# Optimization experiments

Hardware: AMD Instinct MI355X
Metric: run time of the kernel (lower is better)

## Reference

```python
import jax, jax.numpy as jnp
import numpy as np

NUM_HEADS = 24
HEAD_DIM = 128
DIM = NUM_HEADS * HEAD_DIM  # 3072
EPS = 1e-6


def rms_norm(x, g):
    # x: [b, h, s, d], g: [d]
    var = jnp.mean(jnp.square(x.astype(jnp.float32)), axis=-1, keepdims=True)
    return (x.astype(jnp.float32) * jax.lax.rsqrt(var + EPS)).astype(x.dtype) * g


def apply_rope(x, cos, sin):
    # x: [b, h, s, d]; cos/sin: [s, d//2]; complex multiply on interleaved pairs
    b, h, s, d = x.shape
    xr = x.reshape(b, h, s, d // 2, 2)
    x0, x1 = xr[..., 0], xr[..., 1]
    c = cos[None, None, :, :]
    sn = sin[None, None, :, :]
    o0 = x0 * c - x1 * sn
    o1 = x0 * sn + x1 * c
    return jnp.stack([o0, o1], axis=-1).reshape(b, h, s, d)


def split_heads(x):
    # [b, s, h*d] -> [b, h, s, d]
    b, s, _ = x.shape
    return x.reshape(b, s, NUM_HEADS, HEAD_DIM).transpose(0, 2, 1, 3)


def setup_inputs() -> dict:
    key = jax.random.key(0)
    ks = jax.random.split(key, 16)
    b, s_img, s_txt = 1, 2048, 256
    image = jax.random.normal(ks[0], (b, s_img, DIM), jnp.float32)
    text = jax.random.normal(ks[1], (b, s_txt, DIM), jnp.float32)
    # rotary freqs: angles = pos * inv_freq
    half = HEAD_DIM // 2
    inv_freq = 1.0 / (10000.0 ** (np.arange(half, dtype=np.float32) / half))
    ang_i = np.arange(s_img, dtype=np.float32)[:, None] * inv_freq[None, :]
    ang_t = np.arange(s_txt, dtype=np.float32)[:, None] * inv_freq[None, :]
    img_cos, img_sin = jnp.cos(jnp.asarray(ang_i)), jnp.sin(jnp.asarray(ang_i))
    txt_cos, txt_sin = jnp.cos(jnp.asarray(ang_t)), jnp.sin(jnp.asarray(ang_t))
    sc = 1.0 / np.sqrt(DIM)
    Wqkv = jax.random.normal(ks[2], (DIM, 3 * DIM), jnp.float32) * sc
    bqkv = jnp.zeros((3 * DIM,), jnp.float32)
    Wadd = jax.random.normal(ks[3], (DIM, 3 * DIM), jnp.float32) * sc
    badd = jnp.zeros((3 * DIM,), jnp.float32)
    gq = jnp.ones((HEAD_DIM,), jnp.float32)
    gk = jnp.ones((HEAD_DIM,), jnp.float32)
    gaq = jnp.ones((HEAD_DIM,), jnp.float32)
    gak = jnp.ones((HEAD_DIM,), jnp.float32)
    Wout = jax.random.normal(ks[4], (DIM, DIM), jnp.float32) * sc
    bout = jnp.zeros((DIM,), jnp.float32)
    Waddout = jax.random.normal(ks[5], (DIM, DIM), jnp.float32) * sc
    baddout = jnp.zeros((DIM,), jnp.float32)
    return dict(image=image, text=text, img_cos=img_cos, img_sin=img_sin,
                txt_cos=txt_cos, txt_sin=txt_sin, Wqkv=Wqkv, bqkv=bqkv,
                Wadd=Wadd, badd=badd, gq=gq, gk=gk, gaq=gaq, gak=gak,
                Wout=Wout, bout=bout, Waddout=Waddout, baddout=baddout)


def reference(image, text, img_cos, img_sin, txt_cos, txt_sin,
              Wqkv, bqkv, Wadd, badd, gq, gk, gaq, gak,
              Wout, bout, Waddout, baddout):
    seq_txt = text.shape[1]
    img_qkv = image @ Wqkv + bqkv
    img_q, img_k, img_v = jnp.split(img_qkv, 3, axis=-1)
    txt_qkv = text @ Wadd + badd
    txt_q, txt_k, txt_v = jnp.split(txt_qkv, 3, axis=-1)

    img_q, img_k, img_v = split_heads(img_q), split_heads(img_k), split_heads(img_v)
    txt_q, txt_k, txt_v = split_heads(txt_q), split_heads(txt_k), split_heads(txt_v)

    img_q, img_k = rms_norm(img_q, gq), rms_norm(img_k, gk)
    txt_q, txt_k = rms_norm(txt_q, gaq), rms_norm(txt_k, gak)

    img_q = apply_rope(img_q, img_cos, img_sin)
    img_k = apply_rope(img_k, img_cos, img_sin)
    txt_q = apply_rope(txt_q, txt_cos, txt_sin)
    txt_k = apply_rope(txt_k, txt_cos, txt_sin)

    # joint attention: text tokens first, then image tokens
    q = jnp.concatenate([txt_q, img_q], axis=2)  # [b, h, S, d]
    k = jnp.concatenate([txt_k, img_k], axis=2)
    v = jnp.concatenate([txt_v, img_v], axis=2)

    scale = 1.0 / np.sqrt(HEAD_DIM)
    scores = jnp.einsum('bhqd,bhkd->bhqk', q, k) * scale
    probs = jax.nn.softmax(scores, axis=-1)
    attn = jnp.einsum('bhqk,bhkd->bhqd', probs, v)
    b, h, S, d = attn.shape
    attn = attn.transpose(0, 2, 1, 3).reshape(b, S, h * d)  # [b, S, dim]

    txt_out = attn[:, :seq_txt, :]
    img_out = attn[:, seq_txt:, :]
    img_out = img_out @ Wout + bout
    txt_out = txt_out @ Waddout + baddout
    return img_out, txt_out
```

## Files before the change

### kernel.cpp

```cpp
#include <hip/hip_runtime.h>

#define NH 24
#define HD 128
#define DM 3072
#define DM3 9216
#define STXT 256
#define SIMG 2048
#define SALL 2304

typedef __attribute__((ext_vector_type(8))) short bfrag;
typedef __attribute__((ext_vector_type(4))) float ffrag;

__device__ __forceinline__ unsigned short f2bf(float f) {
  unsigned int x = __builtin_bit_cast(unsigned int, f);
  x += 0x7fffu + ((x >> 16) & 1u);
  return (unsigned short)(x >> 16);
}

__device__ __forceinline__ void gload16(void* lds, const void* g) {
  __builtin_amdgcn_global_load_lds((const __attribute__((address_space(1))) unsigned int*)g,
                                   (__attribute__((address_space(3))) unsigned int*)lds, 16, 0, 0);
}

__global__ __launch_bounds__(256) void cast_kernel(const float* __restrict__ in,
                                                   unsigned short* __restrict__ out) {
  int i = blockIdx.x * 256 + threadIdx.x;
  float4 a = ((const float4*)in)[2 * i];
  float4 b = ((const float4*)in)[2 * i + 1];
  uint4 o;
  o.x = (unsigned)f2bf(a.x) | ((unsigned)f2bf(a.y) << 16);
  o.y = (unsigned)f2bf(a.z) | ((unsigned)f2bf(a.w) << 16);
  o.z = (unsigned)f2bf(b.x) | ((unsigned)f2bf(b.y) << 16);
  o.w = (unsigned)f2bf(b.z) | ((unsigned)f2bf(b.w) << 16);
  ((uint4*)out)[i] = o;
}

__global__ __launch_bounds__(256) void transpose_cast_kernel(const float* __restrict__ W,
                                                             unsigned short* __restrict__ Wt,
                                                             int K, int N) {
  __shared__ __align__(16) unsigned short tile[64 * 72];
  int k0 = blockIdx.y * 64, n0 = blockIdx.x * 64;
  int t = threadIdx.x;
  int rr = t >> 4, cc = (t & 15) * 4;
#pragma unroll
  for (int p = 0; p < 4; ++p) {
    int k = rr + p * 16;
    float4 v = *(const float4*)&W[(size_t)(k0 + k) * N + n0 + cc];
    tile[(cc + 0) * 72 + k] = f2bf(v.x);
    tile[(cc + 1) * 72 + k] = f2bf(v.y);
    tile[(cc + 2) * 72 + k] = f2bf(v.z);
    tile[(cc + 3) * 72 + k] = f2bf(v.w);
  }
  __syncthreads();
  int n = t >> 2, c = (t & 3) * 16;
  float4* dst = (float4*)&Wt[(size_t)(n0 + n) * K + k0 + c];
  dst[0] = *(float4*)&tile[n * 72 + c];
  dst[1] = *(float4*)&tile[n * 72 + c + 8];
}

__global__ __launch_bounds__(256) void gemm_bt(const unsigned short* __restrict__ A,
                                               const unsigned short* __restrict__ Bt,
                                               const float* __restrict__ bias,
                                               int M, int N, int K, int mode,
                                               float* __restrict__ outf,
                                               unsigned short* __restrict__ outb, int s_off) {
  __shared__ __align__(16) unsigned short As[128 * 32];
  __shared__ __align__(16) unsigned short Bs[128 * 32];
  const int tid = threadIdx.x;
  const int wave = tid >> 6, lane = tid & 63, quad = lane >> 4, l16 = lane & 15;
  const int wm = (wave >> 1) * 64, wn = (wave & 1) * 64;
  const size_t m0 = (size_t)blockIdx.y * 128, n0 = (size_t)blockIdx.x * 128;

  ffrag zf = {0.f, 0.f, 0.f, 0.f};
  ffrag acc[4][4];
#pragma unroll
  for (int i = 0; i < 4; ++i)
#pragma unroll
    for (int j = 0; j < 4; ++j) acc[i][j] = zf;

  const int sr = tid >> 2;
  const int sc = (tid & 3) * 8;
  const unsigned short* Ag0 = A + (m0 + sr) * K + sc;
  const unsigned short* Bg0 = Bt + (n0 + sr) * K + sc;
  unsigned short* Ad0 = &As[sr * 32 + sc];
  unsigned short* Ad1 = &As[(sr + 64) * 32 + sc];
  unsigned short* Bd0 = &Bs[sr * 32 + sc];
  unsigned short* Bd1 = &Bs[(sr + 64) * 32 + sc];

  for (int k0 = 0; k0 < K; k0 += 32) {
    __syncthreads();
    gload16(Ad0, Ag0 + k0);
    gload16(Ad1, Ag0 + (size_t)64 * K + k0);
    gload16(Bd0, Bg0 + k0);
    gload16(Bd1, Bg0 + (size_t)64 * K + k0);
    __syncthreads();
    bfrag af[4], bfv[4];
#pragma unroll
    for (int mt = 0; mt < 4; ++mt)
      af[mt] = *(const bfrag*)&As[(wm + mt * 16 + l16) * 32 + quad * 8];
#pragma unroll
    for (int nt = 0; nt < 4; ++nt)
      bfv[nt] = *(const bfrag*)&Bs[(wn + nt * 16 + l16) * 32 + quad * 8];
#pragma unroll
    for (int mt = 0; mt < 4; ++mt)
#pragma unroll
      for (int nt = 0; nt < 4; ++nt)
        acc[mt][nt] = __builtin_amdgcn_mfma_f32_16x16x32_bf16(af[mt], bfv[nt], acc[mt][nt], 0, 0, 0);
  }

  float bv[4];
#pragma unroll
  for (int nt = 0; nt < 4; ++nt) bv[nt] = bias[n0 + wn + nt * 16 + l16];

#pragma unroll
  for (int mt = 0; mt < 4; ++mt) {
#pragma unroll
    for (int nt = 0; nt < 4; ++nt) {
      int gn = (int)n0 + wn + nt * 16 + l16;
#pragma unroll
      for (int r = 0; r < 4; ++r) {
        float v = acc[mt][nt][r] + bv[nt];
        int gm = (int)m0 + wm + mt * 16 + quad * 4 + r;
        if (mode == 2) {
          outf[(size_t)gm * N + gn] = v;
        } else {
          int which = gn / DM;
          int rr2 = gn - which * DM;
          int head = rr2 >> 7, d = rr2 & 127;
          int s = s_off + gm;
          if (which < 2)
            outf[(((size_t)which * NH + head) * SALL + s) * HD + d] = v;
          else
            outb[((size_t)head * HD + d) * SALL + s] = f2bf(v);
        }
      }
    }
  }
}

__global__ __launch_bounds__(256) void norm_rope_kernel(
    const float* __restrict__ qkvf, const float* __restrict__ gq, const float* __restrict__ gk,
    const float* __restrict__ gaq, const float* __restrict__ gak,
    const float* __restrict__ img_cos, const float* __restrict__ img_sin,
    const float* __restrict__ txt_cos, const float* __restrict__ txt_sin,
    unsigned short* __restrict__ Qb, unsigned short* __restrict__ Kb) {
  int wave = threadIdx.x >> 6, lane = threadIdx.x & 63;
  int row = blockIdx.x * 4 + wave;
  int which = row / (NH * SALL);
  int rem = row - which * (NH * SALL);
  int s = rem % SALL;
  float2 v = *(const float2*)&qkvf[(size_t)row * HD + lane * 2];
  float ss = v.x * v.x + v.y * v.y;
#pragma unroll
  for (int m = 1; m < 64; m <<= 1) ss += __shfl_xor(ss, m);
  float rinv = rsqrtf(ss * (1.0f / 128.0f) + 1e-6f);
  bool is_txt = s < STXT;
  int pos = is_txt ? s : s - STXT;
  const float* g = (which == 0) ? (is_txt ? gaq : gq) : (is_txt ? gak : gk);
  const float* ct = is_txt ? txt_cos : img_cos;
  const float* st = is_txt ? txt_sin : img_sin;
  float c = ct[pos * 64 + lane], sn = st[pos * 64 + lane];
  float x0 = v.x * rinv * g[lane * 2];
  float x1 = v.y * rinv * g[lane * 2 + 1];
  float o0 = x0 * c - x1 * sn;
  float o1 = x0 * sn + x1 * c;
  unsigned short* out = (which == 0 ? Qb : Kb) + (size_t)rem * HD + lane * 2;
  *(unsigned int*)out = (unsigned)f2bf(o0) | ((unsigned)f2bf(o1) << 16);
}

__global__ __launch_bounds__(256) void flash_kernel(const unsigned short* __restrict__ Q,
                                                    const unsigned short* __restrict__ Kg,
                                                    const unsigned short* __restrict__ Vt,
                                                    unsigned short* __restrict__ attn) {
  __shared__ __align__(16) unsigned short Kl[64 * 128];
  __shared__ __align__(16) unsigned short Vl[128 * 64];
  __shared__ __align__(16) unsigned short Pl[4 * 16 * 64];
  int bid = blockIdx.x;
  int g = (bid & 7) * 108 + (bid >> 3);
  const int h = g / 36;
  const int qb = (g - h * 36) * 64;
  const int tid = threadIdx.x;
  const int wave = tid >> 6, lane = tid & 63, quad = lane >> 4, l16 = lane & 15;
  const int l7 = l16 & 7;

  const unsigned short* qrow = Q + ((size_t)h * SALL + qb + wave * 16 + l16) * HD;
  bfrag aq[4];
#pragma unroll
  for (int kk = 0; kk < 4; ++kk) aq[kk] = *(const bfrag*)&qrow[kk * 32 + quad * 8];

  const unsigned short* Kh = Kg + (size_t)h * SALL * HD;
  const unsigned short* Vh = Vt + (size_t)h * HD * SALL;

  const int kr = tid >> 4, kc = tid & 15;
  const int vr = tid >> 3, vc = tid & 7;
  const int kswz = kc ^ (kr & 7);
  const int vswz = vc ^ (vr & 7);

  ffrag zf = {0.f, 0.f, 0.f, 0.f};
  ffrag o[8];
#pragma unroll
  for (int i = 0; i < 8; ++i) o[i] = zf;
  float m_r[4] = {-__builtin_inff(), -__builtin_inff(), -__builtin_inff(), -__builtin_inff()};
  float l_r[4] = {0.f, 0.f, 0.f, 0.f};
  const float sc = 0.08838834764831845f * 1.4426950408889634f;

  bfrag kreg[4], vreg[4];
#pragma unroll
  for (int p = 0; p < 4; ++p) {
    kreg[p] = *(const bfrag*)&Kh[(size_t)(kr + p * 16) * HD + kc * 8];
    vreg[p] = *(const bfrag*)&Vh[(size_t)(vr + p * 32) * SALL + vc * 8];
  }

  for (int t = 0; t < SALL / 64; ++t) {
    __syncthreads();
#pragma unroll
    for (int p = 0; p < 4; ++p) {
      *(bfrag*)&Kl[(kr + p * 16) * 128 + kswz * 8] = kreg[p];
      *(bfrag*)&Vl[(vr + p * 32) * 64 + vswz * 8] = vreg[p];
    }
    __syncthreads();

    if (t + 1 < SALL / 64) {
      int kn = (t + 1) * 64;
#pragma unroll
      for (int p = 0; p < 4; ++p) {
        kreg[p] = *(const bfrag*)&Kh[(size_t)(kn + kr + p * 16) * HD + kc * 8];
        vreg[p] = *(const bfrag*)&Vh[(size_t)(vr + p * 32) * SALL + kn + vc * 8];
      }
    }

    ffrag s_[4];
#pragma unroll
    for (int nt = 0; nt < 4; ++nt) s_[nt] = zf;
#pragma unroll
    for (int kk = 0; kk < 4; ++kk) {
#pragma unroll
      for (int nt = 0; nt < 4; ++nt) {
        bfrag kf = *(const bfrag*)&Kl[(nt * 16 + l16) * 128 + ((kk * 4 + quad) ^ l7) * 8];
        s_[nt] = __builtin_amdgcn_mfma_f32_16x16x32_bf16(aq[kk], kf, s_[nt], 0, 0, 0);
      }
    }
#pragma unroll
    for (int nt = 0; nt < 4; ++nt)
#pragma unroll
      for (int r = 0; r < 4; ++r) s_[nt][r] *= sc;

    float alpha[4];
#pragma unroll
    for (int r = 0; r < 4; ++r) {
      float mx = fmaxf(fmaxf(s_[0][r], s_[1][r]), fmaxf(s_[2][r], s_[3][r]));
#pragma unroll
      for (int msk = 1; msk < 16; msk <<= 1) mx = fmaxf(mx, __shfl_xor(mx, msk));
      float mnew = fmaxf(m_r[r], mx);
      alpha[r] = exp2f(m_r[r] - mnew);
      m_r[r] = mnew;
      float rs = 0.f;
#pragma unroll
      for (int nt = 0; nt < 4; ++nt) {
        float p = exp2f(s_[nt][r] - mnew);
        s_[nt][r] = p;
        rs += p;
      }
#pragma unroll
      for (int msk = 1; msk < 16; msk <<= 1) rs += __shfl_xor(rs, msk);
      l_r[r] = l_r[r] * alpha[r] + rs;
    }
#pragma unroll
    for (int dt = 0; dt < 8; ++dt)
#pragma unroll
      for (int r = 0; r < 4; ++r) o[dt][r] *= alpha[r];
#pragma unroll
    for (int r = 0; r < 4; ++r) {
      int prow = quad * 4 + r;
#pragma unroll
      for (int nt = 0; nt < 4; ++nt)
        Pl[wave * 1024 + prow * 64 + ((nt * 16 + l16) ^ ((prow & 7) << 3))] = f2bf(s_[nt][r]);
    }

    bfrag pf0 = *(const bfrag*)&Pl[wave * 1024 + l16 * 64 + ((quad)     ^ l7) * 8];
    bfrag pf1 = *(const bfrag*)&Pl[wave * 1024 + l16 * 64 + ((quad + 4) ^ l7) * 8];
#pragma unroll
    for (int dt = 0; dt < 8; ++dt) {
      bfrag vf0 = *(const bfrag*)&Vl[(dt * 16 + l16) * 64 + ((quad)     ^ l7) * 8];
      bfrag vf1 = *(const bfrag*)&Vl[(dt * 16 + l16) * 64 + ((quad + 4) ^ l7) * 8];
      o[dt] = __builtin_amdgcn_mfma_f32_16x16x32_bf16(pf0, vf0, o[dt], 0, 0, 0);
      o[dt] = __builtin_amdgcn_mfma_f32_16x16x32_bf16(pf1, vf1, o[dt], 0, 0, 0);
    }
  }

  float linv[4];
#pragma unroll
  for (int r = 0; r < 4; ++r) linv[r] = 1.0f / l_r[r];
#pragma unroll
  for (int dt = 0; dt < 8; ++dt) {
#pragma unroll
    for (int r = 0; r < 4; ++r) {
      int s = qb + wave * 16 + quad * 4 + r;
      attn[(size_t)s * DM + h * HD + dt * 16 + l16] = f2bf(o[dt][r] * linv[r]);
    }
  }
}

extern "C" void kernel_launch(void* const* d_in, const int* in_sizes, int n_in,
                              void* d_out, int out_size, void* d_ws, size_t ws_size,
                              hipStream_t stream) {
  const float* image = (const float*)d_in[0];
  const float* text = (const float*)d_in[1];
  const float* img_cos = (const float*)d_in[2];
  const float* img_sin = (const float*)d_in[3];
  const float* txt_cos = (const float*)d_in[4];
  const float* txt_sin = (const float*)d_in[5];
  const float* Wqkv = (const float*)d_in[6];
  const float* bqkv = (const float*)d_in[7];
  const float* Wadd = (const float*)d_in[8];
  const float* badd = (const float*)d_in[9];
  const float* gq = (const float*)d_in[10];
  const float* gk = (const float*)d_in[11];
  const float* gaq = (const float*)d_in[12];
  const float* gak = (const float*)d_in[13];
  const float* Wout = (const float*)d_in[14];
  const float* bout = (const float*)d_in[15];
  const float* Waddout = (const float*)d_in[16];
  const float* baddout = (const float*)d_in[17];

  char* ws = (char*)d_ws;
  size_t off = 0;
  unsigned short* img_bf = (unsigned short*)(ws + off); off += (size_t)SIMG * DM * 2;
  unsigned short* txt_bf = (unsigned short*)(ws + off); off += (size_t)STXT * DM * 2;
  unsigned short* attn = img_bf;
  unsigned short* Wqkv_t = (unsigned short*)(ws + off); off += (size_t)DM3 * DM * 2;
  unsigned short* Wadd_t = (unsigned short*)(ws + off); off += (size_t)DM3 * DM * 2;
  unsigned short* Wout_t = (unsigned short*)(ws + off); off += (size_t)DM * DM * 2;
  unsigned short* Waddout_t = (unsigned short*)(ws + off); off += (size_t)DM * DM * 2;
  float* qkvf = (float*)(ws + off); off += (size_t)2 * NH * SALL * HD * 4;
  unsigned short* Qb = (unsigned short*)(ws + off); off += (size_t)NH * SALL * HD * 2;
  unsigned short* Kb = (unsigned short*)(ws + off); off += (size_t)NH * SALL * HD * 2;
  unsigned short* Vtb = (unsigned short*)(ws + off); off += (size_t)NH * HD * SALL * 2;
  if (off > ws_size) return;

  cast_kernel<<<SIMG * DM / 2048, 256, 0, stream>>>(image, img_bf);
  cast_kernel<<<STXT * DM / 2048, 256, 0, stream>>>(text, txt_bf);
  transpose_cast_kernel<<<dim3(DM3 / 64, DM / 64), 256, 0, stream>>>(Wqkv, Wqkv_t, DM, DM3);
  transpose_cast_kernel<<<dim3(DM3 / 64, DM / 64), 256, 0, stream>>>(Wadd, Wadd_t, DM, DM3);
  transpose_cast_kernel<<<dim3(DM / 64, DM / 64), 256, 0, stream>>>(Wout, Wout_t, DM, DM);
  transpose_cast_kernel<<<dim3(DM / 64, DM / 64), 256, 0, stream>>>(Waddout, Waddout_t, DM, DM);

  gemm_bt<<<dim3(DM3 / 128, SIMG / 128), 256, 0, stream>>>(img_bf, Wqkv_t, bqkv, SIMG, DM3, DM,
                                                           0, qkvf, Vtb, STXT);
  gemm_bt<<<dim3(DM3 / 128, STXT / 128), 256, 0, stream>>>(txt_bf, Wadd_t, badd, STXT, DM3, DM,
                                                           0, qkvf, Vtb, 0);

  norm_rope_kernel<<<2 * NH * SALL / 4, 256, 0, stream>>>(qkvf, gq, gk, gaq, gak, img_cos,
                                                          img_sin, txt_cos, txt_sin, Qb, Kb);

  flash_kernel<<<dim3(SALL / 64 * NH), 256, 0, stream>>>(Qb, Kb, Vtb, attn);

  gemm_bt<<<dim3(DM / 128, SIMG / 128), 256, 0, stream>>>(attn + (size_t)STXT * DM, Wout_t, bout,
                                                          SIMG, DM, DM, 2, (float*)d_out, nullptr, 0);
  gemm_bt<<<dim3(DM / 128, STXT / 128), 256, 0, stream>>>(attn, Waddout_t, baddout, STXT, DM, DM,
                                                          2, (float*)d_out + (size_t)SIMG * DM,
                                                          nullptr, 0);
}
```

Measured before the change: 1.031 ms.

## Replace 128x128 GEMM with double-buffered 256x256 tile kernel merging text/image launches

Replaces the 128x128 single-buffered bf16 GEMM with a 512-thread 256x256 tile kernel. It uses a 64-wide K step, double-buffered LDS fills via global_load_lds, a swizzled LDS layout, and interleaved MFMA phases with barriers and setprio. Text and image rows are stored contiguously, so each projection pair runs as one launch: the first 256-row block (text) selects the text weights and bias, and the rest use the image weights. The aim is more operand reuse, overlap of memory loads with MFMA work, and fewer launches. The trade-offs are higher register and LDS pressure and fewer blocks per launch.

```diff
diff --git a/kernel.cpp b/kernel.cpp
--- a/kernel.cpp
+++ b/kernel.cpp
@@ -58,80 +58,154 @@
   dst[1] = *(float4*)&tile[n * 72 + c + 8];
 }
 
-__global__ __launch_bounds__(256) void gemm_bt(const unsigned short* __restrict__ A,
-                                               const unsigned short* __restrict__ Bt,
-                                               const float* __restrict__ bias,
-                                               int M, int N, int K, int mode,
-                                               float* __restrict__ outf,
-                                               unsigned short* __restrict__ outb, int s_off) {
-  __shared__ __align__(16) unsigned short As[128 * 32];
-  __shared__ __align__(16) unsigned short Bs[128 * 32];
+#define STAGE256(tt, c)                                                                          \
+  {                                                                                              \
+    const size_t kof = (size_t)(tt)*64;                                                          \
+    _Pragma("unroll") for (int hf = 0; hf < 2; ++hf) {                                           \
+      _Pragma("unroll") for (int i = 0; i < 2; ++i) {                                            \
+        gload16(&SA[c][hf][i * 4096 + sdst], Asrc + (size_t)(hf * 128 + i * 64) * K + kof);      \
+        gload16(&SB[c][hf][i * 4096 + sdst], Bsrc + (size_t)(hf * 128 + i * 64) * K + kof);      \
+      }                                                                                          \
+    }                                                                                            \
+  }
+
+#define RDA(QM)                                                                       \
+  _Pragma("unroll") for (int mi = 0; mi < 4; ++mi) {                                  \
+    a_[mi * 2 + 0] = *(const bfrag*)&Ab[((QM)*64 + mi * 16 + l16) * 64 + ck0];        \
+    a_[mi * 2 + 1] = *(const bfrag*)&Ab[((QM)*64 + mi * 16 + l16) * 64 + ck1];        \
+  }
+
+#define RDB(QN, DST)                                                                  \
+  _Pragma("unroll") for (int ni = 0; ni < 2; ++ni) {                                  \
+    DST[ni * 2 + 0] = *(const bfrag*)&Bb[((QN)*32 + ni * 16 + l16) * 64 + ck0];       \
+    DST[ni * 2 + 1] = *(const bfrag*)&Bb[((QN)*32 + ni * 16 + l16) * 64 + ck1];       \
+  }
+
+#define MQUAD(QM, QN, BOP)                                                            \
+  _Pragma("unroll") for (int mi = 0; mi < 4; ++mi) {                                  \
+    _Pragma("unroll") for (int ni = 0; ni < 2; ++ni) {                                \
+      _Pragma("unroll") for (int kk = 0; kk < 2; ++kk) {                              \
+        acc[(QM)*4 + mi][(QN)*2 + ni] = __builtin_amdgcn_mfma_f32_16x16x32_bf16(      \
+            a_[mi * 2 + kk], BOP[ni * 2 + kk], acc[(QM)*4 + mi][(QN)*2 + ni], 0, 0, 0); \
+      }                                                                               \
+    }                                                                                 \
+  }
+
+__global__ __launch_bounds__(512, 2) void gemm256(const unsigned short* __restrict__ A,
+                                                  const unsigned short* __restrict__ Bt_txt,
+                                                  const unsigned short* __restrict__ Bt_img,
+                                                  const float* __restrict__ bias_txt,
+                                                  const float* __restrict__ bias_img,
+                                                  int N, int K, int mode,
+                                                  float* __restrict__ qkvf,
+                                                  unsigned short* __restrict__ vtb,
+                                                  float* __restrict__ out_txt,
+                                                  float* __restrict__ out_img) {
+  __shared__ __align__(16) unsigned short SA[2][2][8192];
+  __shared__ __align__(16) unsigned short SB[2][2][8192];
   const int tid = threadIdx.x;
   const int wave = tid >> 6, lane = tid & 63, quad = lane >> 4, l16 = lane & 15;
-  const int wm = (wave >> 1) * 64, wn = (wave & 1) * 64;
-  const size_t m0 = (size_t)blockIdx.y * 128, n0 = (size_t)blockIdx.x * 128;
+  const int wr = wave >> 2, wc = wave & 3;
+  const int m0 = blockIdx.y * 256, n0 = blockIdx.x * 256;
+  const unsigned short* Bt = (m0 == 0) ? Bt_txt : Bt_img;
+  const float* bias = (m0 == 0) ? bias_txt : bias_img;
+
+  const int srow = wave * 8 + (lane >> 3);
+  const int scs = ((lane & 7) ^ (((lane >> 5) & 1) << 1)) * 8;
+  const int sdst = wave * 512 + lane * 8;
+  const unsigned short* Asrc = A + (size_t)(m0 + srow) * K + scs;
+  const unsigned short* Bsrc = Bt + (size_t)(n0 + srow) * K + scs;
+
+  const int aswz = ((l16 >> 2) & 1) << 1;
+  const int ck0 = ((quad)&3 ^ aswz) * 8;
+  const int ck1 = ((quad + 4) ^ aswz) * 8;
 
   ffrag zf = {0.f, 0.f, 0.f, 0.f};
-  ffrag acc[4][4];
-#pragma unroll
-  for (int i = 0; i < 4; ++i)
+  ffrag acc[8][4];
+#pragma unroll
+  for (int i = 0; i < 8; ++i)
 #pragma unroll
     for (int j = 0; j < 4; ++j) acc[i][j] = zf;
 
-  const int sr = tid >> 2;
-  const int sc = (tid & 3) * 8;
-  const unsigned short* Ag0 = A + (m0 + sr) * K + sc;
-  const unsigned short* Bg0 = Bt + (n0 + sr) * K + sc;
-  unsigned short* Ad0 = &As[sr * 32 + sc];
-  unsigned short* Ad1 = &As[(sr + 64) * 32 + sc];
-  unsigned short* Bd0 = &Bs[sr * 32 + sc];
-  unsigned short* Bd1 = &Bs[(sr + 64) * 32 + sc];
-
-  for (int k0 = 0; k0 < K; k0 += 32) {
-    __syncthreads();
-    gload16(Ad0, Ag0 + k0);
-    gload16(Ad1, Ag0 + (size_t)64 * K + k0);
-    gload16(Bd0, Bg0 + k0);
-    gload16(Bd1, Bg0 + (size_t)64 * K + k0);
-    __syncthreads();
-    bfrag af[4], bfv[4];
-#pragma unroll
-    for (int mt = 0; mt < 4; ++mt)
-      af[mt] = *(const bfrag*)&As[(wm + mt * 16 + l16) * 32 + quad * 8];
-#pragma unroll
-    for (int nt = 0; nt < 4; ++nt)
-      bfv[nt] = *(const bfrag*)&Bs[(wn + nt * 16 + l16) * 32 + quad * 8];
-#pragma unroll
-    for (int mt = 0; mt < 4; ++mt)
-#pragma unroll
-      for (int nt = 0; nt < 4; ++nt)
-        acc[mt][nt] = __builtin_amdgcn_mfma_f32_16x16x32_bf16(af[mt], bfv[nt], acc[mt][nt], 0, 0, 0);
-  }
-
-  float bv[4];
-#pragma unroll
-  for (int nt = 0; nt < 4; ++nt) bv[nt] = bias[n0 + wn + nt * 16 + l16];
-
-#pragma unroll
-  for (int mt = 0; mt < 4; ++mt) {
-#pragma unroll
-    for (int nt = 0; nt < 4; ++nt) {
-      int gn = (int)n0 + wn + nt * 16 + l16;
+  const int NT = K >> 6;
+  STAGE256(0, 0);
+  STAGE256(1, 1);
+
+  for (int t = 0; t < NT; ++t) {
+    const int cur = t & 1;
+    if (t + 1 < NT) {
+      asm volatile("s_waitcnt vmcnt(8)" ::: "memory");
+    } else {
+      asm volatile("s_waitcnt vmcnt(0)" ::: "memory");
+    }
+    __builtin_amdgcn_sched_barrier(0);
+    __builtin_amdgcn_s_barrier();
+    __builtin_amdgcn_sched_barrier(0);
+
+    const unsigned short* Ab = &SA[cur][wr][0];
+    const unsigned short* Bb = &SB[cur][wc >> 1][(wc & 1) * 4096];
+    bfrag a_[8], b0_[4], b1_[4];
+
+    RDA(0);
+    RDB(0, b0_);
+    __builtin_amdgcn_s_barrier();
+    asm volatile("s_waitcnt lgkmcnt(0)" ::: "memory");
+    __builtin_amdgcn_sched_barrier(0);
+    __builtin_amdgcn_s_setprio(1);
+    MQUAD(0, 0, b0_);
+    __builtin_amdgcn_s_setprio(0);
+    __builtin_amdgcn_s_barrier();
+
+    RDB(1, b1_);
+    __builtin_amdgcn_s_barrier();
+    asm volatile("s_waitcnt lgkmcnt(0)" ::: "memory");
+    __builtin_amdgcn_sched_barrier(0);
+    __builtin_amdgcn_s_setprio(1);
+    MQUAD(0, 1, b1_);
+    __builtin_amdgcn_s_setprio(0);
+    __builtin_amdgcn_s_barrier();
+
+    RDA(1);
+    __builtin_amdgcn_s_barrier();
+    asm volatile("s_waitcnt lgkmcnt(0)" ::: "memory");
+    __builtin_amdgcn_sched_barrier(0);
+    __builtin_amdgcn_s_setprio(1);
+    MQUAD(1, 0, b0_);
+    __builtin_amdgcn_s_setprio(0);
+    __builtin_amdgcn_s_barrier();
+    __builtin_amdgcn_sched_barrier(0);
+
+    if (t + 2 < NT) STAGE256(t + 2, cur);
+    __builtin_amdgcn_sched_barrier(0);
+    __builtin_amdgcn_s_setprio(1);
+    MQUAD(1, 1, b1_);
+    __builtin_amdgcn_s_setprio(0);
+  }
+
+#pragma unroll
+  for (int a = 0; a < 8; ++a) {
+    const int rowb = m0 + wr * 128 + (a >> 2) * 64 + (a & 3) * 16 + quad * 4;
+#pragma unroll
+    for (int b = 0; b < 4; ++b) {
+      const int gn = n0 + wc * 64 + (b >> 1) * 32 + (b & 1) * 16 + l16;
+      const float bv = bias[gn];
 #pragma unroll
       for (int r = 0; r < 4; ++r) {
-        float v = acc[mt][nt][r] + bv[nt];
-        int gm = (int)m0 + wm + mt * 16 + quad * 4 + r;
+        float v = acc[a][b][r] + bv;
+        int gm = rowb + r;
         if (mode == 2) {
-          outf[(size_t)gm * N + gn] = v;
+          if (gm < STXT)
+            out_txt[(size_t)gm * N + gn] = v;
+          else
+            out_img[(size_t)(gm - STXT) * N + gn] = v;
         } else {
           int which = gn / DM;
           int rr2 = gn - which * DM;
           int head = rr2 >> 7, d = rr2 & 127;
-          int s = s_off + gm;
           if (which < 2)
-            outf[(((size_t)which * NH + head) * SALL + s) * HD + d] = v;
+            qkvf[(((size_t)which * NH + head) * SALL + gm) * HD + d] = v;
           else
-            outb[((size_t)head * HD + d) * SALL + s] = f2bf(v);
+            vtb[((size_t)head * HD + d) * SALL + gm] = f2bf(v);
         }
       }
     }
@@ -325,9 +399,8 @@
 
   char* ws = (char*)d_ws;
   size_t off = 0;
-  unsigned short* img_bf = (unsigned short*)(ws + off); off += (size_t)SIMG * DM * 2;
-  unsigned short* txt_bf = (unsigned short*)(ws + off); off += (size_t)STXT * DM * 2;
-  unsigned short* attn = img_bf;
+  unsigned short* x_bf = (unsigned short*)(ws + off); off += (size_t)SALL * DM * 2;
+  unsigned short* attn = x_bf;
   unsigned short* Wqkv_t = (unsigned short*)(ws + off); off += (size_t)DM3 * DM * 2;
   unsigned short* Wadd_t = (unsigned short*)(ws + off); off += (size_t)DM3 * DM * 2;
   unsigned short* Wout_t = (unsigned short*)(ws + off); off += (size_t)DM * DM * 2;
@@ -338,26 +411,22 @@
   unsigned short* Vtb = (unsigned short*)(ws + off); off += (size_t)NH * HD * SALL * 2;
   if (off > ws_size) return;
 
-  cast_kernel<<<SIMG * DM / 2048, 256, 0, stream>>>(image, img_bf);
-  cast_kernel<<<STXT * DM / 2048, 256, 0, stream>>>(text, txt_bf);
+  cast_kernel<<<STXT * DM / 2048, 256, 0, stream>>>(text, x_bf);
+  cast_kernel<<<SIMG * DM / 2048, 256, 0, stream>>>(image, x_bf + (size_t)STXT * DM);
   transpose_cast_kernel<<<dim3(DM3 / 64, DM / 64), 256, 0, stream>>>(Wqkv, Wqkv_t, DM, DM3);
   transpose_cast_kernel<<<dim3(DM3 / 64, DM / 64), 256, 0, stream>>>(Wadd, Wadd_t, DM, DM3);
   transpose_cast_kernel<<<dim3(DM / 64, DM / 64), 256, 0, stream>>>(Wout, Wout_t, DM, DM);
   transpose_cast_kernel<<<dim3(DM / 64, DM / 64), 256, 0, stream>>>(Waddout, Waddout_t, DM, DM);
 
-  gemm_bt<<<dim3(DM3 / 128, SIMG / 128), 256, 0, stream>>>(img_bf, Wqkv_t, bqkv, SIMG, DM3, DM,
-                                                           0, qkvf, Vtb, STXT);
-  gemm_bt<<<dim3(DM3 / 128, STXT / 128), 256, 0, stream>>>(txt_bf, Wadd_t, badd, STXT, DM3, DM,
-                                                           0, qkvf, Vtb, 0);
+  gemm256<<<dim3(DM3 / 256, SALL / 256), 512, 0, stream>>>(
+      x_bf, Wadd_t, Wqkv_t, badd, bqkv, DM3, DM, 0, qkvf, Vtb, nullptr, nullptr);
 
   norm_rope_kernel<<<2 * NH * SALL / 4, 256, 0, stream>>>(qkvf, gq, gk, gaq, gak, img_cos,
                                                           img_sin, txt_cos, txt_sin, Qb, Kb);
 
   flash_kernel<<<dim3(SALL / 64 * NH), 256, 0, stream>>>(Qb, Kb, Vtb, attn);
 
-  gemm_bt<<<dim3(DM / 128, SIMG / 128), 256, 0, stream>>>(attn + (size_t)STXT * DM, Wout_t, bout,
-                                                          SIMG, DM, DM, 2, (float*)d_out, nullptr, 0);
-  gemm_bt<<<dim3(DM / 128, STXT / 128), 256, 0, stream>>>(attn, Waddout_t, baddout, STXT, DM, DM,
-                                                          2, (float*)d_out + (size_t)SIMG * DM,
-                                                          nullptr, 0);
-}
+  gemm256<<<dim3(DM / 256, SALL / 256), 512, 0, stream>>>(
+      attn, Waddout_t, Wout_t, baddout, bout, DM, DM, 2, nullptr, nullptr,
+      (float*)d_out + (size_t)SIMG * DM, (float*)d_out);
+}
```

Result: faster. 0.9997 ms (-3.0%).

## Merge text/image GEMMs into one launch with LDS double buffering and XCD swizzle

Applied to the files above, without the earlier changes.

Text and image activations are cast into one contiguous buffer, so each projection pair (QKV and output) runs as a single GEMM launch that picks weights and bias per 128-row tile. The GEMM main loop now double-buffers LDS, issuing the next tile's global-to-LDS loads before computing the current one, which leaves one barrier per k-step instead of two. Block IDs are remapped so consecutive tiles land on the same XCD for better L2 reuse. This removes two launches and the small underfilled text GEMMs, and overlaps loads with MFMA, at the cost of doubling LDS use per block.

```diff
diff --git a/kernel.cpp b/kernel.cpp
--- a/kernel.cpp
+++ b/kernel.cpp
@@ -58,18 +58,53 @@
   dst[1] = *(float4*)&tile[n * 72 + c + 8];
 }
 
-__global__ __launch_bounds__(256) void gemm_bt(const unsigned short* __restrict__ A,
-                                               const unsigned short* __restrict__ Bt,
-                                               const float* __restrict__ bias,
-                                               int M, int N, int K, int mode,
-                                               float* __restrict__ outf,
-                                               unsigned short* __restrict__ outb, int s_off) {
-  __shared__ __align__(16) unsigned short As[128 * 32];
-  __shared__ __align__(16) unsigned short Bs[128 * 32];
+#define STG128(TT, CB)                                                    \
+  {                                                                       \
+    const size_t kof = (size_t)(TT)*32;                                   \
+    gload16(&As[CB][sr * 32 + sc], Ag + kof);                             \
+    gload16(&As[CB][(sr + 64) * 32 + sc], Ag + (size_t)64 * K + kof);     \
+    gload16(&Bs[CB][sr * 32 + sc], Bg + kof);                             \
+    gload16(&Bs[CB][(sr + 64) * 32 + sc], Bg + (size_t)64 * K + kof);     \
+  }
+
+#define TILE128(TT, CB)                                                               \
+  {                                                                                   \
+    if ((TT) + 1 < NT) STG128((TT) + 1, (CB) ^ 1);                                    \
+    bfrag af[4], bfv[4];                                                              \
+    _Pragma("unroll") for (int mt = 0; mt < 4; ++mt)                                  \
+        af[mt] = *(const bfrag*)&As[CB][(wm + mt * 16 + l16) * 32 + quad * 8];        \
+    _Pragma("unroll") for (int nt = 0; nt < 4; ++nt)                                  \
+        bfv[nt] = *(const bfrag*)&Bs[CB][(wn + nt * 16 + l16) * 32 + quad * 8];       \
+    _Pragma("unroll") for (int mt = 0; mt < 4; ++mt)                                  \
+        _Pragma("unroll") for (int nt = 0; nt < 4; ++nt)                              \
+            acc[mt][nt] =                                                             \
+                __builtin_amdgcn_mfma_f32_16x16x32_bf16(af[mt], bfv[nt], acc[mt][nt], \
+                                                        0, 0, 0);                     \
+    __syncthreads();                                                                  \
+  }
+
+__global__ __launch_bounds__(256) void gemm128(const unsigned short* __restrict__ A,
+                                               const unsigned short* __restrict__ Bt_txt,
+                                               const unsigned short* __restrict__ Bt_img,
+                                               const float* __restrict__ bias_txt,
+                                               const float* __restrict__ bias_img,
+                                               int N, int K, int ncols, int mode,
+                                               float* __restrict__ qkvf,
+                                               unsigned short* __restrict__ vtb,
+                                               float* __restrict__ out_txt,
+                                               float* __restrict__ out_img) {
+  __shared__ __align__(16) unsigned short As[2][128 * 32];
+  __shared__ __align__(16) unsigned short Bs[2][128 * 32];
   const int tid = threadIdx.x;
   const int wave = tid >> 6, lane = tid & 63, quad = lane >> 4, l16 = lane & 15;
   const int wm = (wave >> 1) * 64, wn = (wave & 1) * 64;
-  const size_t m0 = (size_t)blockIdx.y * 128, n0 = (size_t)blockIdx.x * 128;
+  const int nwg = gridDim.x;
+  const int q8 = nwg >> 3, r8 = nwg & 7;
+  const int xcd = blockIdx.x & 7, idx = blockIdx.x >> 3;
+  const int wg = (xcd < r8 ? xcd * (q8 + 1) : r8 * (q8 + 1) + (xcd - r8) * q8) + idx;
+  const int m0 = (wg / ncols) * 128, n0 = (wg % ncols) * 128;
+  const unsigned short* Bt = (m0 < STXT) ? Bt_txt : Bt_img;
+  const float* bias = (m0 < STXT) ? bias_txt : bias_img;
 
   ffrag zf = {0.f, 0.f, 0.f, 0.f};
   ffrag acc[4][4];
@@ -80,32 +115,15 @@
 
   const int sr = tid >> 2;
   const int sc = (tid & 3) * 8;
-  const unsigned short* Ag0 = A + (m0 + sr) * K + sc;
-  const unsigned short* Bg0 = Bt + (n0 + sr) * K + sc;
-  unsigned short* Ad0 = &As[sr * 32 + sc];
-  unsigned short* Ad1 = &As[(sr + 64) * 32 + sc];
-  unsigned short* Bd0 = &Bs[sr * 32 + sc];
-  unsigned short* Bd1 = &Bs[(sr + 64) * 32 + sc];
-
-  for (int k0 = 0; k0 < K; k0 += 32) {
-    __syncthreads();
-    gload16(Ad0, Ag0 + k0);
-    gload16(Ad1, Ag0 + (size_t)64 * K + k0);
-    gload16(Bd0, Bg0 + k0);
-    gload16(Bd1, Bg0 + (size_t)64 * K + k0);
-    __syncthreads();
-    bfrag af[4], bfv[4];
-#pragma unroll
-    for (int mt = 0; mt < 4; ++mt)
-      af[mt] = *(const bfrag*)&As[(wm + mt * 16 + l16) * 32 + quad * 8];
-#pragma unroll
-    for (int nt = 0; nt < 4; ++nt)
-      bfv[nt] = *(const bfrag*)&Bs[(wn + nt * 16 + l16) * 32 + quad * 8];
-#pragma unroll
-    for (int mt = 0; mt < 4; ++mt)
-#pragma unroll
-      for (int nt = 0; nt < 4; ++nt)
-        acc[mt][nt] = __builtin_amdgcn_mfma_f32_16x16x32_bf16(af[mt], bfv[nt], acc[mt][nt], 0, 0, 0);
+  const unsigned short* Ag = A + (size_t)(m0 + sr) * K + sc;
+  const unsigned short* Bg = Bt + (size_t)(n0 + sr) * K + sc;
+
+  const int NT = K >> 5;
+  STG128(0, 0);
+  __syncthreads();
+  for (int t = 0; t < NT; t += 2) {
+    TILE128(t, 0);
+    TILE128(t + 1, 1);
   }
 
   float bv[4];
@@ -122,16 +140,18 @@
         float v = acc[mt][nt][r] + bv[nt];
         int gm = (int)m0 + wm + mt * 16 + quad * 4 + r;
         if (mode == 2) {
-          outf[(size_t)gm * N + gn] = v;
+          if (gm < STXT)
+            out_txt[(size_t)gm * N + gn] = v;
+          else
+            out_img[(size_t)(gm - STXT) * N + gn] = v;
         } else {
           int which = gn / DM;
           int rr2 = gn - which * DM;
           int head = rr2 >> 7, d = rr2 & 127;
-          int s = s_off + gm;
           if (which < 2)
-            outf[(((size_t)which * NH + head) * SALL + s) * HD + d] = v;
+            qkvf[(((size_t)which * NH + head) * SALL + gm) * HD + d] = v;
           else
-            outb[((size_t)head * HD + d) * SALL + s] = f2bf(v);
+            vtb[((size_t)head * HD + d) * SALL + gm] = f2bf(v);
         }
       }
     }
@@ -325,9 +345,8 @@
 
   char* ws = (char*)d_ws;
   size_t off = 0;
-  unsigned short* img_bf = (unsigned short*)(ws + off); off += (size_t)SIMG * DM * 2;
-  unsigned short* txt_bf = (unsigned short*)(ws + off); off += (size_t)STXT * DM * 2;
-  unsigned short* attn = img_bf;
+  unsigned short* x_bf = (unsigned short*)(ws + off); off += (size_t)SALL * DM * 2;
+  unsigned short* attn = x_bf;
   unsigned short* Wqkv_t = (unsigned short*)(ws + off); off += (size_t)DM3 * DM * 2;
   unsigned short* Wadd_t = (unsigned short*)(ws + off); off += (size_t)DM3 * DM * 2;
   unsigned short* Wout_t = (unsigned short*)(ws + off); off += (size_t)DM * DM * 2;
@@ -338,26 +357,22 @@
   unsigned short* Vtb = (unsigned short*)(ws + off); off += (size_t)NH * HD * SALL * 2;
   if (off > ws_size) return;
 
-  cast_kernel<<<SIMG * DM / 2048, 256, 0, stream>>>(image, img_bf);
-  cast_kernel<<<STXT * DM / 2048, 256, 0, stream>>>(text, txt_bf);
+  cast_kernel<<<STXT * DM / 2048, 256, 0, stream>>>(text, x_bf);
+  cast_kernel<<<SIMG * DM / 2048, 256, 0, stream>>>(image, x_bf + (size_t)STXT * DM);
   transpose_cast_kernel<<<dim3(DM3 / 64, DM / 64), 256, 0, stream>>>(Wqkv, Wqkv_t, DM, DM3);
   transpose_cast_kernel<<<dim3(DM3 / 64, DM / 64), 256, 0, stream>>>(Wadd, Wadd_t, DM, DM3);
   transpose_cast_kernel<<<dim3(DM / 64, DM / 64), 256, 0, stream>>>(Wout, Wout_t, DM, DM);
   transpose_cast_kernel<<<dim3(DM / 64, DM / 64), 256, 0, stream>>>(Waddout, Waddout_t, DM, DM);
 
-  gemm_bt<<<dim3(DM3 / 128, SIMG / 128), 256, 0, stream>>>(img_bf, Wqkv_t, bqkv, SIMG, DM3, DM,
-                                                           0, qkvf, Vtb, STXT);
-  gemm_bt<<<dim3(DM3 / 128, STXT / 128), 256, 0, stream>>>(txt_bf, Wadd_t, badd, STXT, DM3, DM,
-                                                           0, qkvf, Vtb, 0);
+  gemm128<<<dim3((DM3 / 128) * (SALL / 128)), 256, 0, stream>>>(
+      x_bf, Wadd_t, Wqkv_t, badd, bqkv, DM3, DM, DM3 / 128, 0, qkvf, Vtb, nullptr, nullptr);
 
   norm_rope_kernel<<<2 * NH * SALL / 4, 256, 0, stream>>>(qkvf, gq, gk, gaq, gak, img_cos,
                                                           img_sin, txt_cos, txt_sin, Qb, Kb);
 
   flash_kernel<<<dim3(SALL / 64 * NH), 256, 0, stream>>>(Qb, Kb, Vtb, attn);
 
-  gemm_bt<<<dim3(DM / 128, SIMG / 128), 256, 0, stream>>>(attn + (size_t)STXT * DM, Wout_t, bout,
-                                                          SIMG, DM, DM, 2, (float*)d_out, nullptr, 0);
-  gemm_bt<<<dim3(DM / 128, STXT / 128), 256, 0, stream>>>(attn, Waddout_t, baddout, STXT, DM, DM,
-                                                          2, (float*)d_out + (size_t)SIMG * DM,
-                                                          nullptr, 0);
-}
+  gemm128<<<dim3((DM / 128) * (SALL / 128)), 256, 0, stream>>>(
+      attn, Waddout_t, Wout_t, baddout, bout, DM, DM, DM / 128, 2, nullptr, nullptr,
+      (float*)d_out + (size_t)SIMG * DM, (float*)d_out);
+}
```

New measurement: 863.0 us. -16.3%, faster.
